# Kernel optimization log

Measured on AMD Instinct MI355X. Metric: run time of the kernel, lower is better.

The kernel has to match this reference:

```python
import jax, jax.numpy as jnp
import numpy as np

D_MODEL = 1024
NUM_HEADS = 16
HEAD_DIM = D_MODEL // NUM_HEADS


def setup_inputs() -> dict:
    key = jax.random.key(0)
    ks = jax.random.split(key, 9)
    s = 1.0 / np.sqrt(D_MODEL)
    inp = {
        "x": jax.random.normal(ks[0], (4, 2048, D_MODEL), dtype=jnp.float32),
        "wq": jax.random.uniform(ks[1], (D_MODEL, D_MODEL), jnp.float32, -s, s),
        "bq": jax.random.uniform(ks[2], (D_MODEL,), jnp.float32, -s, s),
        "wk": jax.random.uniform(ks[3], (D_MODEL, D_MODEL), jnp.float32, -s, s),
        "bk": jax.random.uniform(ks[4], (D_MODEL,), jnp.float32, -s, s),
        "wv": jax.random.uniform(ks[5], (D_MODEL, D_MODEL), jnp.float32, -s, s),
        "bv": jax.random.uniform(ks[6], (D_MODEL,), jnp.float32, -s, s),
        "wo": jax.random.uniform(ks[7], (D_MODEL, D_MODEL), jnp.float32, -s, s),
        "bo": jax.random.uniform(ks[8], (D_MODEL,), jnp.float32, -s, s),
    }
    return inp


def _split_heads(t):
    # [B, S, D] -> [B, H, S, Dh]
    b, s, _ = t.shape
    return t.reshape(b, s, NUM_HEADS, HEAD_DIM).transpose(0, 2, 1, 3)


def reference(x, wq, bq, wk, bk, wv, bv, wo, bo):
    b, s, _ = x.shape
    q = _split_heads(x @ wq.T + bq)
    k = _split_heads(x @ wk.T + bk)
    v = _split_heads(x @ wv.T + bv)
    scale = 1.0 / np.sqrt(HEAD_DIM).astype(np.float32)
    scores = jnp.einsum('bhqd,bhkd->bhqk', q, k) * scale  # [B,H,S,S]
    probs = jax.nn.softmax(scores, axis=-1)
    ctx = jnp.einsum('bhqk,bhkd->bhqd', probs, v)  # [B,H,S,Dh]
    ctx = ctx.transpose(0, 2, 1, 3).reshape(b, s, D_MODEL)
    return ctx @ wo.T + bo
```

## Files before the change

kernel.cpp:

```cpp
#include <hip/hip_runtime.h>
#include <stdint.h>

typedef short bf16x8 __attribute__((ext_vector_type(8)));
typedef float f32x4 __attribute__((ext_vector_type(4)));

#define D_MODEL 1024
#define NHEAD   16
#define HDIM    64
#define BATCH   4
#define SEQ     2048
#define NTOK    (BATCH * SEQ)

#define BM 128
#define BN 128
#define BK 64

#define LOG2E 1.44269504088896340736f

__device__ __forceinline__ unsigned short f2bf(float f) {
  unsigned int u = __float_as_uint(f);
  u += 0x7fff + ((u >> 16) & 1);
  return (unsigned short)(u >> 16);
}

__device__ __forceinline__ void gload_lds16(const unsigned short* g, unsigned short* l) {
  __builtin_amdgcn_global_load_lds((const __attribute__((address_space(1))) void*)g,
                                   (__attribute__((address_space(3))) void*)l,
                                   16, 0, 0);
}

__global__ __launch_bounds__(256) void cvt_all(
    const float* __restrict__ x, const float* __restrict__ wq,
    const float* __restrict__ wk, const float* __restrict__ wv,
    const float* __restrict__ wo, unsigned short* __restrict__ dst) {
  long i = ((long)blockIdx.x * 256 + threadIdx.x) * 4;
  const float* src; long off;
  if (i < 8388608)       { src = x;  off = 0; }
  else if (i < 9437184)  { src = wq; off = 8388608; }
  else if (i < 10485760) { src = wk; off = 9437184; }
  else if (i < 11534336) { src = wv; off = 10485760; }
  else                   { src = wo; off = 11534336; }
  const float4 v = *(const float4*)(src + (i - off));
  ushort4 o = make_ushort4(f2bf(v.x), f2bf(v.y), f2bf(v.z), f2bf(v.w));
  *(ushort4*)(dst + i) = o;
}

__device__ __forceinline__ void gemm_bt_mainloop(
    const unsigned short* __restrict__ Abase,
    const unsigned short* __restrict__ Bbase,
    int lda, int ldb, int K,
    unsigned short* sA, unsigned short* sB,
    f32x4 acc[4][4]) {
  const int tid = threadIdx.x;
  const int wave = tid >> 6, lane = tid & 63;
  const int ln15 = lane & 15, quad = lane >> 4;
  const int wy = wave >> 1, wx = wave & 1;

#pragma unroll
  for (int mt = 0; mt < 4; ++mt)
#pragma unroll
    for (int nt = 0; nt < 4; ++nt)
      acc[mt][nt] = (f32x4){0.f, 0.f, 0.f, 0.f};

  for (int k0 = 0; k0 < K; k0 += BK) {
    __syncthreads();
#pragma unroll
    for (int i = 0; i < 4; ++i) {
      int chunk = i * 256 + wave * 64 + lane;
      int row = chunk >> 3, c = (chunk & 7) ^ (row & 7);
      gload_lds16(Abase + row * lda + k0 + c * 8, sA + (i * 256 + wave * 64) * 8);
      gload_lds16(Bbase + row * ldb + k0 + c * 8, sB + (i * 256 + wave * 64) * 8);
    }
    __syncthreads();
#pragma unroll
    for (int ks = 0; ks < 2; ++ks) {
      const int swz = ((ks * 4 + quad) ^ (ln15 & 7)) * 8;
      bf16x8 af[4], bfv[4];
#pragma unroll
      for (int t = 0; t < 4; ++t)
        af[t] = *(const bf16x8*)(sA + (64 * wy + 16 * t + ln15) * BK + swz);
#pragma unroll
      for (int t = 0; t < 4; ++t)
        bfv[t] = *(const bf16x8*)(sB + (64 * wx + 16 * t + ln15) * BK + swz);
#pragma unroll
      for (int mt = 0; mt < 4; ++mt)
#pragma unroll
        for (int nt = 0; nt < 4; ++nt)
          acc[mt][nt] = __builtin_amdgcn_mfma_f32_16x16x32_bf16(af[mt], bfv[nt], acc[mt][nt], 0, 0, 0);
    }
  }
}

#define TSTR 136
__global__ __launch_bounds__(256) void qkv_gemm(
    const unsigned short* __restrict__ xb,
    const unsigned short* __restrict__ wqb, const unsigned short* __restrict__ wkb,
    const unsigned short* __restrict__ wvb,
    const float* __restrict__ bq, const float* __restrict__ bk, const float* __restrict__ bv,
    unsigned short* __restrict__ Qb, unsigned short* __restrict__ Kb,
    unsigned short* __restrict__ Vt) {
  const int z = blockIdx.z;
  const unsigned short* W = (z == 0) ? wqb : (z == 1) ? wkb : wvb;
  const float* bias = (z == 0) ? bq : (z == 1) ? bk : bv;
  const int m0 = blockIdx.x * BM, n0 = blockIdx.y * BN;

  __shared__ __align__(16) unsigned char smem[BM * TSTR * 2];
  unsigned short* sA = (unsigned short*)smem;
  unsigned short* sB = (unsigned short*)(smem + BM * BK * 2);
  unsigned short* sT = (unsigned short*)smem;

  f32x4 acc[4][4];
  gemm_bt_mainloop(xb + (size_t)m0 * D_MODEL, W + (size_t)n0 * D_MODEL,
                   D_MODEL, D_MODEL, D_MODEL, sA, sB, acc);

  const int tid = threadIdx.x;
  const int lane = tid & 63, wave = tid >> 6;
  const int ln15 = lane & 15, quad = lane >> 4;
  const int wy = wave >> 1, wx = wave & 1;

  if (z == 2) {
    __syncthreads();
#pragma unroll
    for (int mt = 0; mt < 4; ++mt)
#pragma unroll
      for (int nt = 0; nt < 4; ++nt) {
        int j = 64 * wx + 16 * nt + ln15;
        float bj = bias[n0 + j];
#pragma unroll
        for (int r = 0; r < 4; r += 2) {
          int tok = 64 * wy + 16 * mt + quad * 4 + r;
          unsigned int pk = (unsigned int)f2bf(acc[mt][nt][r]) |
                            ((unsigned int)f2bf(acc[mt][nt][r + 1]) << 16);
          pk = (unsigned int)f2bf(acc[mt][nt][r] + bj) |
               ((unsigned int)f2bf(acc[mt][nt][r + 1] + bj) << 16);
          *(unsigned int*)(sT + j * TSTR + tok) = pk;
        }
      }
    __syncthreads();
    const int b = m0 >> 11;
    const int sbase = (m0 & 2047) + (tid & 15) * 8;
#pragma unroll
    for (int i = 0; i < 8; ++i) {
      int j = (tid >> 4) + i * 16;
      int feature = n0 + j;
      int h = feature >> 6, d = feature & 63;
      bf16x8 val = *(const bf16x8*)(sT + j * TSTR + (tid & 15) * 8);
      *(bf16x8*)(Vt + (((size_t)(b * NHEAD + h)) * HDIM + d) * SEQ + sbase) = val;
    }
  } else {
    const float scale = (z == 0) ? 0.125f * LOG2E : 1.0f;
    unsigned short* dst = (z == 0) ? Qb : Kb;
#pragma unroll
    for (int mt = 0; mt < 4; ++mt)
#pragma unroll
      for (int nt = 0; nt < 4; ++nt)
#pragma unroll
        for (int r = 0; r < 4; ++r) {
          int n = m0 + 64 * wy + 16 * mt + quad * 4 + r;
          int j = n0 + 64 * wx + 16 * nt + ln15;
          float v = (acc[mt][nt][r] + bias[j]) * scale;
          int b = n >> 11, s = n & 2047, h = j >> 6, d = j & 63;
          dst[(((size_t)(b * NHEAD + h)) * SEQ + s) * HDIM + d] = f2bf(v);
        }
  }
}

#define PSTR 72
__global__ __launch_bounds__(256, 4) void attn_kernel(
    const unsigned short* __restrict__ Qb,
    const unsigned short* __restrict__ Kb,
    const unsigned short* __restrict__ Vt,
    unsigned short* __restrict__ ctxb) {
  const int qb = blockIdx.x;
  const int bh = blockIdx.y;
  const int s0 = qb * 128;
  const int tid = threadIdx.x, wave = tid >> 6, lane = tid & 63;
  const int ln15 = lane & 15, quad = lane >> 4;

  __shared__ __align__(16) unsigned short sK[64 * 64], sV[64 * 64], sP[128 * PSTR];

  const unsigned short* Qg = Qb + (size_t)bh * SEQ * HDIM;
  const unsigned short* Kg = Kb + (size_t)bh * SEQ * HDIM;
  const unsigned short* Vg = Vt + (size_t)bh * HDIM * SEQ;

  bf16x8 qf[2][2];
#pragma unroll
  for (int mt = 0; mt < 2; ++mt)
#pragma unroll
    for (int ks = 0; ks < 2; ++ks)
      qf[mt][ks] = *(const bf16x8*)(Qg + (s0 + 32 * wave + 16 * mt + ln15) * HDIM + ks * 32 + quad * 8);

  const int chunk0 = wave * 64 + lane;
  const int row0 = chunk0 >> 3, c0 = (chunk0 & 7) ^ (row0 & 7);
  const int chunk1 = 256 + wave * 64 + lane;
  const int row1 = chunk1 >> 3, c1 = (chunk1 & 7) ^ (row1 & 7);
  const unsigned short* Kp0 = Kg + row0 * HDIM + c0 * 8;
  const unsigned short* Kp1 = Kg + row1 * HDIM + c1 * 8;
  const unsigned short* Vp0 = Vg + row0 * SEQ + c0 * 8;
  const unsigned short* Vp1 = Vg + row1 * SEQ + c1 * 8;
  unsigned short* dK0 = sK + (wave * 64) * 8;
  unsigned short* dK1 = sK + (256 + wave * 64) * 8;
  unsigned short* dV0 = sV + (wave * 64) * 8;
  unsigned short* dV1 = sV + (256 + wave * 64) * 8;

  float l_part[8];
  f32x4 O[2][4];
#pragma unroll
  for (int i = 0; i < 8; ++i) l_part[i] = 0.f;
#pragma unroll
  for (int mt = 0; mt < 2; ++mt)
#pragma unroll
    for (int dt = 0; dt < 4; ++dt) O[mt][dt] = (f32x4){0.f, 0.f, 0.f, 0.f};

  for (int k0 = 0; k0 < SEQ; k0 += 64) {
    __syncthreads();
    gload_lds16(Kp0 + k0 * HDIM, dK0);
    gload_lds16(Kp1 + k0 * HDIM, dK1);
    gload_lds16(Vp0 + k0, dV0);
    gload_lds16(Vp1 + k0, dV1);
    __syncthreads();

    f32x4 sc[2][4];
#pragma unroll
    for (int mt = 0; mt < 2; ++mt)
#pragma unroll
      for (int nt = 0; nt < 4; ++nt) sc[mt][nt] = (f32x4){0.f, 0.f, 0.f, 0.f};
#pragma unroll
    for (int ks = 0; ks < 2; ++ks) {
      const int swz = ((ks * 4 + quad) ^ (ln15 & 7)) * 8;
#pragma unroll
      for (int nt = 0; nt < 4; ++nt) {
        bf16x8 bk8 = *(const bf16x8*)(sK + (16 * nt + ln15) * 64 + swz);
#pragma unroll
        for (int mt = 0; mt < 2; ++mt)
          sc[mt][nt] = __builtin_amdgcn_mfma_f32_16x16x32_bf16(qf[mt][ks], bk8, sc[mt][nt], 0, 0, 0);
      }
    }

#pragma unroll
    for (int mt = 0; mt < 2; ++mt)
#pragma unroll
      for (int r = 0; r < 4; ++r) {
        float p0 = __builtin_amdgcn_exp2f(sc[mt][0][r]);
        float p1 = __builtin_amdgcn_exp2f(sc[mt][1][r]);
        float p2 = __builtin_amdgcn_exp2f(sc[mt][2][r]);
        float p3 = __builtin_amdgcn_exp2f(sc[mt][3][r]);
        l_part[mt * 4 + r] += (p0 + p1) + (p2 + p3);
        int prow = 32 * wave + 16 * mt + quad * 4 + r;
        sP[prow * PSTR + 0  + ln15] = f2bf(p0);
        sP[prow * PSTR + 16 + ln15] = f2bf(p1);
        sP[prow * PSTR + 32 + ln15] = f2bf(p2);
        sP[prow * PSTR + 48 + ln15] = f2bf(p3);
      }

#pragma unroll
    for (int ks = 0; ks < 2; ++ks) {
      const int swz = ((ks * 4 + quad) ^ (ln15 & 7)) * 8;
      bf16x8 ap[2];
#pragma unroll
      for (int mt = 0; mt < 2; ++mt)
        ap[mt] = *(const bf16x8*)(sP + (32 * wave + 16 * mt + ln15) * PSTR + ks * 32 + quad * 8);
#pragma unroll
      for (int dt = 0; dt < 4; ++dt) {
        bf16x8 bv8 = *(const bf16x8*)(sV + (16 * dt + ln15) * 64 + swz);
#pragma unroll
        for (int mt = 0; mt < 2; ++mt)
          O[mt][dt] = __builtin_amdgcn_mfma_f32_16x16x32_bf16(ap[mt], bv8, O[mt][dt], 0, 0, 0);
      }
    }
  }

  const int b = bh >> 4, h = bh & 15;
#pragma unroll
  for (int mt = 0; mt < 2; ++mt)
#pragma unroll
    for (int r = 0; r < 4; ++r) {
      float l = l_part[mt * 4 + r];
      l += __shfl_xor(l, 1);
      l += __shfl_xor(l, 2);
      l += __shfl_xor(l, 4);
      l += __shfl_xor(l, 8);
      float inv = 1.0f / l;
      int token = b * SEQ + s0 + 32 * wave + 16 * mt + quad * 4 + r;
#pragma unroll
      for (int dt = 0; dt < 4; ++dt)
        ctxb[(size_t)token * D_MODEL + h * HDIM + 16 * dt + ln15] = f2bf(O[mt][dt][r] * inv);
    }
}

__global__ __launch_bounds__(256) void oproj_kernel(
    const unsigned short* __restrict__ ctxb,
    const unsigned short* __restrict__ wob,
    const float* __restrict__ bo,
    float* __restrict__ out) {
  const int m0 = blockIdx.x * BM, n0 = blockIdx.y * BN;
  __shared__ __align__(16) unsigned short sA[BM * BK], sB[BN * BK];
  f32x4 acc[4][4];
  gemm_bt_mainloop(ctxb + (size_t)m0 * D_MODEL, wob + (size_t)n0 * D_MODEL,
                   D_MODEL, D_MODEL, D_MODEL, sA, sB, acc);

  const int lane = threadIdx.x & 63, wave = threadIdx.x >> 6;
  const int ln15 = lane & 15, quad = lane >> 4;
  const int wy = wave >> 1, wx = wave & 1;
#pragma unroll
  for (int mt = 0; mt < 4; ++mt)
#pragma unroll
    for (int nt = 0; nt < 4; ++nt)
#pragma unroll
      for (int r = 0; r < 4; ++r) {
        int n = m0 + 64 * wy + 16 * mt + quad * 4 + r;
        int j = n0 + 64 * wx + 16 * nt + ln15;
        out[(size_t)n * D_MODEL + j] = acc[mt][nt][r] + bo[j];
      }
}

extern "C" void kernel_launch(void* const* d_in, const int* in_sizes, int n_in,
                              void* d_out, int out_size, void* d_ws, size_t ws_size,
                              hipStream_t stream) {
  const float* x  = (const float*)d_in[0];
  const float* wq = (const float*)d_in[1];
  const float* bq = (const float*)d_in[2];
  const float* wk = (const float*)d_in[3];
  const float* bk = (const float*)d_in[4];
  const float* wv = (const float*)d_in[5];
  const float* bv = (const float*)d_in[6];
  const float* wo = (const float*)d_in[7];
  const float* bo = (const float*)d_in[8];
  float* out = (float*)d_out;

  unsigned short* ws   = (unsigned short*)d_ws;
  unsigned short* xb   = ws;
  unsigned short* Qb   = ws + 12582912;
  unsigned short* Kb   = ws + 20971520;
  unsigned short* Vtb  = ws + 29360128;
  unsigned short* ctxb = ws + 37748736;
  unsigned short* wqb  = ws + 8388608;
  unsigned short* wkb  = ws + 9437184;
  unsigned short* wvb  = ws + 10485760;
  unsigned short* wob  = ws + 11534336;

  cvt_all<<<12288, 256, 0, stream>>>(x, wq, wk, wv, wo, ws);

  qkv_gemm<<<dim3(64, 8, 3), 256, 0, stream>>>(xb, wqb, wkb, wvb, bq, bk, bv, Qb, Kb, Vtb);
  attn_kernel<<<dim3(16, 64), 256, 0, stream>>>(Qb, Kb, Vtb, ctxb);
  oproj_kernel<<<dim3(64, 8), 256, 0, stream>>>(ctxb, wob, bo, out);
}
```

Measured before the change: 284.0 us.

## Stage Q/K epilogue through LDS and register-prefetch K/V tiles in attention

The Q/K projection epilogue now writes results into shared memory and then issues coalesced 16-byte stores per head row, instead of scattered 2-byte global stores. Bias values are hoisted into registers. In the attention kernel, direct global-to-LDS loads are replaced by register prefetch of the next K/V tile, stored to LDS at the top of each iteration, so global latency can overlap with the MFMA work. It also drops a redundant dead bf16 pack in the V epilogue. The prefetch costs extra registers, which may reduce occupancy.

```diff
diff --git a/kernel.cpp b/kernel.cpp
--- a/kernel.cpp
+++ b/kernel.cpp
@@ -117,6 +117,7 @@
   const int lane = tid & 63, wave = tid >> 6;
   const int ln15 = lane & 15, quad = lane >> 4;
   const int wy = wave >> 1, wx = wave & 1;
+  const int b = m0 >> 11;
 
   if (z == 2) {
     __syncthreads();
@@ -129,15 +130,12 @@
 #pragma unroll
         for (int r = 0; r < 4; r += 2) {
           int tok = 64 * wy + 16 * mt + quad * 4 + r;
-          unsigned int pk = (unsigned int)f2bf(acc[mt][nt][r]) |
-                            ((unsigned int)f2bf(acc[mt][nt][r + 1]) << 16);
-          pk = (unsigned int)f2bf(acc[mt][nt][r] + bj) |
-               ((unsigned int)f2bf(acc[mt][nt][r + 1] + bj) << 16);
+          unsigned int pk = (unsigned int)f2bf(acc[mt][nt][r] + bj) |
+                            ((unsigned int)f2bf(acc[mt][nt][r + 1] + bj) << 16);
           *(unsigned int*)(sT + j * TSTR + tok) = pk;
         }
       }
     __syncthreads();
-    const int b = m0 >> 11;
     const int sbase = (m0 & 2047) + (tid & 15) * 8;
 #pragma unroll
     for (int i = 0; i < 8; ++i) {
@@ -150,18 +148,31 @@
   } else {
     const float scale = (z == 0) ? 0.125f * LOG2E : 1.0f;
     unsigned short* dst = (z == 0) ? Qb : Kb;
+    __syncthreads();
+    float bj[4];
+#pragma unroll
+    for (int nt = 0; nt < 4; ++nt) bj[nt] = bias[n0 + 64 * wx + 16 * nt + ln15];
 #pragma unroll
     for (int mt = 0; mt < 4; ++mt)
 #pragma unroll
       for (int nt = 0; nt < 4; ++nt)
 #pragma unroll
         for (int r = 0; r < 4; ++r) {
-          int n = m0 + 64 * wy + 16 * mt + quad * 4 + r;
-          int j = n0 + 64 * wx + 16 * nt + ln15;
-          float v = (acc[mt][nt][r] + bias[j]) * scale;
-          int b = n >> 11, s = n & 2047, h = j >> 6, d = j & 63;
-          dst[(((size_t)(b * NHEAD + h)) * SEQ + s) * HDIM + d] = f2bf(v);
+          int tok = 64 * wy + 16 * mt + quad * 4 + r;
+          int j = 64 * wx + 16 * nt + ln15;
+          sT[tok * TSTR + j] = f2bf((acc[mt][nt][r] + bj[nt]) * scale);
         }
+    __syncthreads();
+    const int srow = m0 & 2047;
+#pragma unroll
+    for (int i = 0; i < 8; ++i) {
+      int tok = (tid >> 4) + i * 16;
+      int jj = (tid & 15) * 8;
+      bf16x8 val = *(const bf16x8*)(sT + tok * TSTR + jj);
+      int feature = n0 + jj;
+      int h = feature >> 6, d = feature & 63;
+      *(bf16x8*)(dst + (((size_t)(b * NHEAD + h)) * SEQ + srow + tok) * HDIM + d) = val;
+    }
   }
 }
 
@@ -198,10 +209,10 @@
   const unsigned short* Kp1 = Kg + row1 * HDIM + c1 * 8;
   const unsigned short* Vp0 = Vg + row0 * SEQ + c0 * 8;
   const unsigned short* Vp1 = Vg + row1 * SEQ + c1 * 8;
-  unsigned short* dK0 = sK + (wave * 64) * 8;
-  unsigned short* dK1 = sK + (256 + wave * 64) * 8;
-  unsigned short* dV0 = sV + (wave * 64) * 8;
-  unsigned short* dV1 = sV + (256 + wave * 64) * 8;
+  unsigned short* dK0 = sK + chunk0 * 8;
+  unsigned short* dK1 = sK + chunk1 * 8;
+  unsigned short* dV0 = sV + chunk0 * 8;
+  unsigned short* dV1 = sV + chunk1 * 8;
 
   float l_part[8];
   f32x4 O[2][4];
@@ -212,13 +223,25 @@
 #pragma unroll
     for (int dt = 0; dt < 4; ++dt) O[mt][dt] = (f32x4){0.f, 0.f, 0.f, 0.f};
 
-  for (int k0 = 0; k0 < SEQ; k0 += 64) {
-    __syncthreads();
-    gload_lds16(Kp0 + k0 * HDIM, dK0);
-    gload_lds16(Kp1 + k0 * HDIM, dK1);
-    gload_lds16(Vp0 + k0, dV0);
-    gload_lds16(Vp1 + k0, dV1);
-    __syncthreads();
+  bf16x8 pk0 = *(const bf16x8*)Kp0;
+  bf16x8 pk1 = *(const bf16x8*)Kp1;
+  bf16x8 pv0 = *(const bf16x8*)Vp0;
+  bf16x8 pv1 = *(const bf16x8*)Vp1;
+
+  for (int t = 0; t < 32; ++t) {
+    __syncthreads();
+    *(bf16x8*)dK0 = pk0;
+    *(bf16x8*)dK1 = pk1;
+    *(bf16x8*)dV0 = pv0;
+    *(bf16x8*)dV1 = pv1;
+    __syncthreads();
+    if (t < 31) {
+      const int k0 = (t + 1) * 64;
+      pk0 = *(const bf16x8*)(Kp0 + k0 * HDIM);
+      pk1 = *(const bf16x8*)(Kp1 + k0 * HDIM);
+      pv0 = *(const bf16x8*)(Vp0 + k0);
+      pv1 = *(const bf16x8*)(Vp1 + k0);
+    }
 
     f32x4 sc[2][4];
 #pragma unroll
@@ -330,14 +353,14 @@
 
   unsigned short* ws   = (unsigned short*)d_ws;
   unsigned short* xb   = ws;
+  unsigned short* wqb  = ws + 8388608;
+  unsigned short* wkb  = ws + 9437184;
+  unsigned short* wvb  = ws + 10485760;
+  unsigned short* wob  = ws + 11534336;
   unsigned short* Qb   = ws + 12582912;
   unsigned short* Kb   = ws + 20971520;
   unsigned short* Vtb  = ws + 29360128;
   unsigned short* ctxb = ws + 37748736;
-  unsigned short* wqb  = ws + 8388608;
-  unsigned short* wkb  = ws + 9437184;
-  unsigned short* wvb  = ws + 10485760;
-  unsigned short* wob  = ws + 11534336;
 
   cvt_all<<<12288, 256, 0, stream>>>(x, wq, wk, wv, wo, ws);
 
```

Result: no change. 280.0 us (-1.4%).
